# Kernel tuning notes

Hardware: AMD Instinct MI355X
Metric: run time of the kernel (lower is better)

Reference implementation:

```python
import jax, jax.numpy as jnp
import numpy as np

CIN, COUT, K = 64, 64, 3
ALPHA = 8.3
STRIDE, PAD, DIL = 1, 1, 1
B, H = 8, 128


def _unfold(x, k, dilation, padding, stride):
    # torch.nn.functional.unfold: output feature order is (C, kh, kw)
    x = jnp.pad(x, ((0, 0), (0, 0), (padding, padding), (padding, padding)))
    b, c, h, w = x.shape
    eff = dilation * (k - 1) + 1
    oh = (h - eff) // stride + 1
    ow = (w - eff) // stride + 1
    cols = []
    for i in range(k):
        for j in range(k):
            cols.append(x[:, :, i * dilation:i * dilation + stride * oh:stride,
                              j * dilation:j * dilation + stride * ow:stride])
    p = jnp.stack(cols, axis=2)          # [B, C, k*k, oh, ow]
    return p.reshape(b, c * k * k, oh * ow)


def setup_inputs() -> dict:
    key = jax.random.key(0)
    k1, k2, k3, k4 = jax.random.split(key, 4)
    image = jax.random.normal(k1, (B, CIN, H, H), dtype=jnp.float32)
    depth = jax.random.uniform(k2, (B, 1, H, H), dtype=jnp.float32)
    weight = jax.random.normal(k3, (COUT, CIN, K, K), dtype=jnp.float32) * 0.05
    bias = jax.random.normal(k4, (COUT,), dtype=jnp.float32) * 0.05
    return {"image": image, "depth": depth, "weight": weight, "bias": bias}


def reference(image, depth, weight, bias):
    # im2col of the image: [B, L, Cin*k*k]
    patches = _unfold(image, K, DIL, PAD, STRIDE).transpose(0, 2, 1)
    b, L, _ = patches.shape
    # depth is repeat()'d to Cin channels in the original; the unfolded depth
    # columns therefore tile the single-channel patch Cin times. Exploit that:
    dpatch = _unfold(depth, K, DIL, PAD, STRIDE).transpose(0, 2, 1)  # [B, L, k*k]
    # original centre index: int((Cin*k*k)/2); within the tiled patch this is
    # position (Cin*k*k//2) % (k*k) of the single-channel patch
    centre_idx = (CIN * K * K // 2) % (K * K)
    centre = dpatch[:, :, centre_idx:centre_idx + 1]
    sim = jnp.exp(-ALPHA * jnp.abs(dpatch - centre))  # [B, L, k*k]
    # modulate per kernel offset (broadcast over channels == tiled similarity)
    modulated = patches.reshape(b, L, CIN, K * K) * sim[:, :, None, :]
    out = jnp.einsum('blck,ock->blo', modulated, weight.reshape(COUT, CIN, K * K))
    out = out + bias
    osz = (image.shape[-1] + 2 * PAD - DIL * (K - 1) - 1) // STRIDE + 1
    return out.transpose(0, 2, 1).reshape(b, COUT, osz, osz)
```

## Files before the change

### kernel.cpp

```cpp
#include <hip/hip_runtime.h>
#include <hip/hip_bf16.h>

#define BATCH 8
#define CIN   64
#define COUT  64
#define HH    128
#define WW    128
#define HW    (HH * WW)
#define ALPHA 8.3f
#define TPX   64
#define YPB   2
#define XW    66

typedef __attribute__((ext_vector_type(8))) short short8;
typedef __attribute__((ext_vector_type(4))) float f32x4;

__device__ __forceinline__ int img_idx(int r, int x, int c) {
    return (((r * XW + x) << 6) + c) ^ ((x & 7) << 3);
}

__global__ __launch_bounds__(256)
void transpose_w(const float* __restrict__ w, __hip_bfloat16* __restrict__ wt) {
    int i = blockIdx.x * 256 + threadIdx.x;
    if (i >= 9 * 64 * 64) return;
    int c = i & 63;
    int o = (i >> 6) & 63;
    int tap = i >> 12;
    wt[i] = __float2bfloat16(w[(o * 64 + c) * 9 + tap]);
}

__global__ __launch_bounds__(256)
void depthconv_fused(const float* __restrict__ image,
                     const float* __restrict__ depth,
                     const float* __restrict__ bias,
                     const short* __restrict__ wt,
                     float* __restrict__ out) {
    __shared__ short s_img[4 * XW * 64];
    __shared__ float s_d[4][XW];
    __shared__ float s_sim[YPB][9][TPX];

    const int tid = threadIdx.x;
    const int bid = blockIdx.x;
    const int yg = bid & 63;
    const int xt = (bid >> 6) & 1;
    const int b  = bid >> 7;
    const int x0 = xt * TPX;
    const int y0 = yg * YPB;

    const int lane = tid & 63;
    const int wid  = tid >> 6;
    const int l15  = lane & 15;
    const int lq   = lane >> 4;
    const int o_base = wid * 16;

    short8 wfrag[9][2];
    #pragma unroll
    for (int tap = 0; tap < 9; ++tap)
        #pragma unroll
        for (int h = 0; h < 2; ++h)
            wfrag[tap][h] = *(const short8*)&wt[(tap * 64 + o_base + l15) * 64 + h * 32 + lq * 8];

    float bias_v[4];
    #pragma unroll
    for (int r = 0; r < 4; ++r) bias_v[r] = bias[o_base + lq * 4 + r];

    {
        const int sx  = 1 + (tid & 63);
        const int srr = tid >> 6;
        const int gy  = y0 - 1 + srr;
        const int gx  = x0 + (tid & 63);
        const bool yok = (unsigned)gy < HH;
        const float* ip = &image[((b * CIN) * HH + gy) * WW + gx];
        const int base = (srr * XW + sx) << 6;
        const int swz  = (sx & 7) << 3;
        #pragma unroll 16
        for (int c2 = 0; c2 < 32; ++c2) {
            float v0 = 0.f, v1 = 0.f;
            if (yok) { v0 = ip[0]; v1 = ip[HW]; }
            ip += 2 * HW;
            __hip_bfloat162 pk = __float22bfloat162_rn(float2{v0, v1});
            *(__hip_bfloat162*)&s_img[base + ((2 * c2) ^ swz)] = pk;
        }
    }
    {
        const int e   = tid & 1;
        const int sx  = e ? (XW - 1) : 0;
        const int rr  = (tid >> 1) & 3;
        const int c2  = tid >> 3;
        const int gy  = y0 - 1 + rr;
        const int gx  = x0 - 1 + sx;
        float v0 = 0.f, v1 = 0.f;
        if ((unsigned)gy < HH && (unsigned)gx < WW) {
            const float* p = &image[((b * CIN + 2 * c2) * HH + gy) * WW + gx];
            v0 = p[0]; v1 = p[HW];
        }
        __hip_bfloat162 pk = __float22bfloat162_rn(float2{v0, v1});
        *(__hip_bfloat162*)&s_img[img_idx(rr, sx, 2 * c2)] = pk;
    }
    for (int i = tid; i < 4 * XW; i += 256) {
        int rr = i / XW, x = i - rr * XW;
        int gy = y0 - 1 + rr, gx = x0 - 1 + x;
        float v = 0.f;
        if ((unsigned)gy < HH && (unsigned)gx < WW)
            v = depth[(b * HH + gy) * WW + gx];
        s_d[rr][x] = v;
    }
    __syncthreads();

    for (int i = tid; i < YPB * 9 * TPX; i += 256) {
        int p  = i & 63;
        int t  = i >> 6;
        int yy = t / 9, tap = t - yy * 9;
        int ri = tap / 3, dj = tap - ri * 3;
        float dt = s_d[yy + ri][p + dj];
        float dc = s_d[yy][p];
        s_sim[yy][tap][p] = __expf(-ALPHA * fabsf(dt - dc));
    }
    __syncthreads();

    #pragma unroll
    for (int nt = 0; nt < 4; ++nt) {
        const int xb = nt * 16 + l15;
        f32x4 a0 = f32x4{0.f, 0.f, 0.f, 0.f};
        f32x4 a1 = f32x4{0.f, 0.f, 0.f, 0.f};

        #pragma unroll
        for (int r = 0; r < 4; ++r) {
            short8 bb[3][2];
            #pragma unroll
            for (int dj = 0; dj < 3; ++dj) {
                bb[dj][0] = *(const short8*)&s_img[img_idx(r, xb + dj, lq * 8)];
                bb[dj][1] = *(const short8*)&s_img[img_idx(r, xb + dj, 32 + lq * 8)];
            }
            if (r < 3) {
                #pragma unroll
                for (int dj = 0; dj < 3; ++dj) {
                    const int tap = 3 * r + dj;
                    f32x4 tmp = __builtin_amdgcn_mfma_f32_16x16x32_bf16(
                        wfrag[tap][0], bb[dj][0], (f32x4){0.f, 0.f, 0.f, 0.f}, 0, 0, 0);
                    tmp = __builtin_amdgcn_mfma_f32_16x16x32_bf16(
                        wfrag[tap][1], bb[dj][1], tmp, 0, 0, 0);
                    const float sv = s_sim[0][tap][xb];
                    #pragma unroll
                    for (int e = 0; e < 4; ++e) a0[e] = fmaf(sv, tmp[e], a0[e]);
                }
            }
            if (r >= 1) {
                #pragma unroll
                for (int dj = 0; dj < 3; ++dj) {
                    const int tap = 3 * (r - 1) + dj;
                    f32x4 tmp = __builtin_amdgcn_mfma_f32_16x16x32_bf16(
                        wfrag[tap][0], bb[dj][0], (f32x4){0.f, 0.f, 0.f, 0.f}, 0, 0, 0);
                    tmp = __builtin_amdgcn_mfma_f32_16x16x32_bf16(
                        wfrag[tap][1], bb[dj][1], tmp, 0, 0, 0);
                    const float sv = s_sim[1][tap][xb];
                    #pragma unroll
                    for (int e = 0; e < 4; ++e) a1[e] = fmaf(sv, tmp[e], a1[e]);
                }
            }
        }

        const int px = x0 + xb;
        #pragma unroll
        for (int rr = 0; rr < 4; ++rr) {
            const int o = o_base + lq * 4 + rr;
            out[((b * COUT + o) * HH + y0) * WW + px]     = a0[rr] + bias_v[rr];
            out[((b * COUT + o) * HH + y0 + 1) * WW + px] = a1[rr] + bias_v[rr];
        }
    }
}

extern "C" void kernel_launch(void* const* d_in, const int* in_sizes, int n_in,
                              void* d_out, int out_size, void* d_ws, size_t ws_size,
                              hipStream_t stream) {
    const float* image  = (const float*)d_in[0];
    const float* depth  = (const float*)d_in[1];
    const float* weight = (const float*)d_in[2];
    const float* bias   = (const float*)d_in[3];
    float* out = (float*)d_out;
    __hip_bfloat16* wt = (__hip_bfloat16*)d_ws;

    transpose_w<<<(9 * 64 * 64 + 255) / 256, 256, 0, stream>>>(weight, wt);

    dim3 grid(BATCH * (HH / YPB) * (WW / TPX));
    depthconv_fused<<<grid, 256, 0, stream>>>(image, depth, bias,
                                              (const short*)wt, out);
}
```

Before: 121.5 us.

## Pre-transpose image to padded NHWC bf16 in workspace and read B-fragments from global

A new prep kernel converts the NCHW fp32 image into a zero-padded channels-last bf16 tensor in workspace, fused with the weight transpose in one launch. The main kernel drops its LDS image staging and reads MFMA B-fragments directly from this global buffer as contiguous 16-byte loads. This removes strided NCHW gathers and shared-memory writes from the main kernel, but adds a full extra pass over the image and relies on L2/cache for the overlapping row reuse across blocks.

```diff
diff --git a/kernel.cpp b/kernel.cpp
--- a/kernel.cpp
+++ b/kernel.cpp
@@ -11,31 +11,61 @@
 #define TPX   64
 #define YPB   2
 #define XW    66
+#define YP    (HH + 2)
+#define XP    (WW + 2)
+
+#define IMGT_SHORTS (BATCH * YP * XP * 64)
+#define WS_NEED_B   ((IMGT_SHORTS + 9 * 64 * 64) * 2)
 
 typedef __attribute__((ext_vector_type(8))) short short8;
 typedef __attribute__((ext_vector_type(4))) float f32x4;
 
-__device__ __forceinline__ int img_idx(int r, int x, int c) {
-    return (((r * XW + x) << 6) + c) ^ ((x & 7) << 3);
+__global__ __launch_bounds__(256)
+void prep(const float* __restrict__ image, const float* __restrict__ weight,
+          __hip_bfloat16* __restrict__ ws) {
+    const int bid = blockIdx.x, tid = threadIdx.x;
+    if (bid < BATCH * YP) {
+        const int b = bid / YP, yp = bid - b * YP;
+        __hip_bfloat16* row = ws + (size_t)(b * YP + yp) * XP * 64;
+        if (yp == 0 || yp == YP - 1) {
+            uint2* p = (uint2*)row;
+            for (int j = tid; j < XP * 64 / 4; j += 256) p[j] = uint2{0u, 0u};
+        } else {
+            __shared__ __hip_bfloat16 s[WW][66];
+            const int gy = yp - 1;
+            const int c0 = tid >> 7;
+            const int gx = tid & 127;
+            const float* ip = image + ((size_t)(b * CIN + c0) * HH + gy) * WW + gx;
+            #pragma unroll
+            for (int cc = 0; cc < 32; ++cc) {
+                s[gx][cc * 2 + c0] = __float2bfloat16(ip[0]);
+                ip += 2 * HW;
+            }
+            __syncthreads();
+            if (tid < 64) {
+                const int e = tid >> 5, cp = (tid & 31) * 2;
+                ((unsigned*)row)[((e ? (XP - 1) : 0) * 64 + cp) >> 1] = 0u;
+            }
+            for (int j = tid; j < WW * 64 / 2; j += 256) {
+                const int o = j * 2;
+                const int xl = o >> 6, c = o & 63;
+                unsigned v = *(const unsigned*)&s[xl][c];
+                *(unsigned*)&row[64 + o] = v;
+            }
+        }
+    } else {
+        const int i = (bid - BATCH * YP) * 256 + tid;
+        const int c = i & 63, o = (i >> 6) & 63, tap = i >> 12;
+        ws[IMGT_SHORTS + i] = __float2bfloat16(weight[(o * 64 + c) * 9 + tap]);
+    }
 }
 
 __global__ __launch_bounds__(256)
-void transpose_w(const float* __restrict__ w, __hip_bfloat16* __restrict__ wt) {
-    int i = blockIdx.x * 256 + threadIdx.x;
-    if (i >= 9 * 64 * 64) return;
-    int c = i & 63;
-    int o = (i >> 6) & 63;
-    int tap = i >> 12;
-    wt[i] = __float2bfloat16(w[(o * 64 + c) * 9 + tap]);
-}
-
-__global__ __launch_bounds__(256)
-void depthconv_fused(const float* __restrict__ image,
-                     const float* __restrict__ depth,
-                     const float* __restrict__ bias,
-                     const short* __restrict__ wt,
-                     float* __restrict__ out) {
-    __shared__ short s_img[4 * XW * 64];
+void depthconv_main(const short* __restrict__ imgT,
+                    const float* __restrict__ depth,
+                    const float* __restrict__ bias,
+                    const short* __restrict__ wt,
+                    float* __restrict__ out) {
     __shared__ float s_d[4][XW];
     __shared__ float s_sim[YPB][9][TPX];
 
@@ -64,39 +94,6 @@
     #pragma unroll
     for (int r = 0; r < 4; ++r) bias_v[r] = bias[o_base + lq * 4 + r];
 
-    {
-        const int sx  = 1 + (tid & 63);
-        const int srr = tid >> 6;
-        const int gy  = y0 - 1 + srr;
-        const int gx  = x0 + (tid & 63);
-        const bool yok = (unsigned)gy < HH;
-        const float* ip = &image[((b * CIN) * HH + gy) * WW + gx];
-        const int base = (srr * XW + sx) << 6;
-        const int swz  = (sx & 7) << 3;
-        #pragma unroll 16
-        for (int c2 = 0; c2 < 32; ++c2) {
-            float v0 = 0.f, v1 = 0.f;
-            if (yok) { v0 = ip[0]; v1 = ip[HW]; }
-            ip += 2 * HW;
-            __hip_bfloat162 pk = __float22bfloat162_rn(float2{v0, v1});
-            *(__hip_bfloat162*)&s_img[base + ((2 * c2) ^ swz)] = pk;
-        }
-    }
-    {
-        const int e   = tid & 1;
-        const int sx  = e ? (XW - 1) : 0;
-        const int rr  = (tid >> 1) & 3;
-        const int c2  = tid >> 3;
-        const int gy  = y0 - 1 + rr;
-        const int gx  = x0 - 1 + sx;
-        float v0 = 0.f, v1 = 0.f;
-        if ((unsigned)gy < HH && (unsigned)gx < WW) {
-            const float* p = &image[((b * CIN + 2 * c2) * HH + gy) * WW + gx];
-            v0 = p[0]; v1 = p[HW];
-        }
-        __hip_bfloat162 pk = __float22bfloat162_rn(float2{v0, v1});
-        *(__hip_bfloat162*)&s_img[img_idx(rr, sx, 2 * c2)] = pk;
-    }
     for (int i = tid; i < 4 * XW; i += 256) {
         int rr = i / XW, x = i - rr * XW;
         int gy = y0 - 1 + rr, gx = x0 - 1 + x;
@@ -106,7 +103,6 @@
         s_d[rr][x] = v;
     }
     __syncthreads();
-
     for (int i = tid; i < YPB * 9 * TPX; i += 256) {
         int p  = i & 63;
         int t  = i >> 6;
@@ -121,6 +117,7 @@
     #pragma unroll
     for (int nt = 0; nt < 4; ++nt) {
         const int xb = nt * 16 + l15;
+        const short* p = imgT + ((size_t)(b * YP + y0) * XP + (x0 + xb)) * 64 + lq * 8;
         f32x4 a0 = f32x4{0.f, 0.f, 0.f, 0.f};
         f32x4 a1 = f32x4{0.f, 0.f, 0.f, 0.f};
 
@@ -129,8 +126,8 @@
             short8 bb[3][2];
             #pragma unroll
             for (int dj = 0; dj < 3; ++dj) {
-                bb[dj][0] = *(const short8*)&s_img[img_idx(r, xb + dj, lq * 8)];
-                bb[dj][1] = *(const short8*)&s_img[img_idx(r, xb + dj, 32 + lq * 8)];
+                bb[dj][0] = *(const short8*)(p + dj * 64);
+                bb[dj][1] = *(const short8*)(p + dj * 64 + 32);
             }
             if (r < 3) {
                 #pragma unroll
@@ -158,6 +155,7 @@
                     for (int e = 0; e < 4; ++e) a1[e] = fmaf(sv, tmp[e], a1[e]);
                 }
             }
+            p += XP * 64;
         }
 
         const int px = x0 + xb;
@@ -178,11 +176,11 @@
     const float* weight = (const float*)d_in[2];
     const float* bias   = (const float*)d_in[3];
     float* out = (float*)d_out;
-    __hip_bfloat16* wt = (__hip_bfloat16*)d_ws;
+    __hip_bfloat16* ws = (__hip_bfloat16*)d_ws;
 
-    transpose_w<<<(9 * 64 * 64 + 255) / 256, 256, 0, stream>>>(weight, wt);
+    prep<<<BATCH * YP + (9 * 64 * 64) / 256, 256, 0, stream>>>(image, weight, ws);
 
     dim3 grid(BATCH * (HH / YPB) * (WW / TPX));
-    depthconv_fused<<<grid, 256, 0, stream>>>(image, depth, bias,
-                                              (const short*)wt, out);
+    depthconv_main<<<grid, 256, 0, stream>>>((const short*)ws, depth, bias,
+                                             (const short*)ws + IMGT_SHORTS, out);
 }
```

Measured after the change: 145.5 us. 19.8% more time.

## Process four output rows per block and prefetch extra halo rows into registers

Applied to the files above, without the earlier changes.

Each block now computes four output rows instead of two, so the one-row halo above and below is shared across more outputs and the redundant image rows loaded into LDS drop. The two extra input rows are loaded into registers before the first compute pass and written to shared memory only after it, overlapping that global load latency with MFMA work. Global loads also become unconditional, with out-of-range values masked afterward. In exchange the grid halves to 512 blocks, LDS use grows, and the 32 staged floats per thread raise register pressure, which may reduce occupancy.

```diff
diff --git a/kernel.cpp b/kernel.cpp
--- a/kernel.cpp
+++ b/kernel.cpp
@@ -9,7 +9,6 @@
 #define HW    (HH * WW)
 #define ALPHA 8.3f
 #define TPX   64
-#define YPB   2
 #define XW    66
 
 typedef __attribute__((ext_vector_type(8))) short short8;
@@ -35,17 +34,17 @@
                      const float* __restrict__ bias,
                      const short* __restrict__ wt,
                      float* __restrict__ out) {
-    __shared__ short s_img[4 * XW * 64];
-    __shared__ float s_d[4][XW];
-    __shared__ float s_sim[YPB][9][TPX];
+    __shared__ short s_img[6 * XW * 64];
+    __shared__ float s_d[6][XW];
+    __shared__ float s_sim[4][9][TPX];
 
     const int tid = threadIdx.x;
     const int bid = blockIdx.x;
-    const int yg = bid & 63;
-    const int xt = (bid >> 6) & 1;
-    const int b  = bid >> 7;
+    const int yg = bid & 31;
+    const int xt = (bid >> 5) & 1;
+    const int b  = bid >> 6;
     const int x0 = xt * TPX;
-    const int y0 = yg * YPB;
+    const int y0 = yg * 4;
 
     const int lane = tid & 63;
     const int wid  = tid >> 6;
@@ -70,13 +69,13 @@
         const int gy  = y0 - 1 + srr;
         const int gx  = x0 + (tid & 63);
         const bool yok = (unsigned)gy < HH;
-        const float* ip = &image[((b * CIN) * HH + gy) * WW + gx];
+        const float* ip = &image[((b * CIN) * HH + (yok ? gy : 0)) * WW + gx];
         const int base = (srr * XW + sx) << 6;
         const int swz  = (sx & 7) << 3;
         #pragma unroll 16
         for (int c2 = 0; c2 < 32; ++c2) {
-            float v0 = 0.f, v1 = 0.f;
-            if (yok) { v0 = ip[0]; v1 = ip[HW]; }
+            float v0 = ip[0], v1 = ip[HW];
+            if (!yok) { v0 = 0.f; v1 = 0.f; }
             ip += 2 * HW;
             __hip_bfloat162 pk = __float22bfloat162_rn(float2{v0, v1});
             *(__hip_bfloat162*)&s_img[base + ((2 * c2) ^ swz)] = pk;
@@ -97,7 +96,7 @@
         __hip_bfloat162 pk = __float22bfloat162_rn(float2{v0, v1});
         *(__hip_bfloat162*)&s_img[img_idx(rr, sx, 2 * c2)] = pk;
     }
-    for (int i = tid; i < 4 * XW; i += 256) {
+    for (int i = tid; i < 6 * XW; i += 256) {
         int rr = i / XW, x = i - rr * XW;
         int gy = y0 - 1 + rr, gx = x0 - 1 + x;
         float v = 0.f;
@@ -105,9 +104,35 @@
             v = depth[(b * HH + gy) * WW + gx];
         s_d[rr][x] = v;
     }
+
+    float st[32];
+    float st_e;
+    const int r45  = 4 + (tid >> 7);
+    const int sx45 = 1 + ((tid >> 1) & 63);
+    const int ch0  = (tid & 1) * 32;
+    {
+        const int gy  = y0 - 1 + r45;
+        const bool ok = (unsigned)gy < HH;
+        const int gx  = x0 + ((tid >> 1) & 63);
+        const float* ip = &image[((size_t)(b * CIN + ch0) * HH + (ok ? gy : 0)) * WW + gx];
+        #pragma unroll
+        for (int c = 0; c < 32; ++c) {
+            float v = ip[0];
+            st[c] = ok ? v : 0.f;
+            ip += HW;
+        }
+        const int ee  = (tid >> 6) & 1;
+        const int ec  = tid & 63;
+        const int gye = y0 - 1 + r45;
+        const int gxe = x0 - 1 + (ee ? 65 : 0);
+        const bool oke = (unsigned)gye < HH && (unsigned)gxe < WW;
+        const float* pe = &image[((size_t)(b * CIN + ec) * HH + (oke ? gye : 0)) * WW + (oke ? gxe : 0)];
+        float ve = pe[0];
+        st_e = oke ? ve : 0.f;
+    }
     __syncthreads();
 
-    for (int i = tid; i < YPB * 9 * TPX; i += 256) {
+    for (int i = tid; i < 4 * 9 * TPX; i += 256) {
         int p  = i & 63;
         int t  = i >> 6;
         int yy = t / 9, tap = t - yy * 9;
@@ -118,56 +143,77 @@
     }
     __syncthreads();
 
-    #pragma unroll
-    for (int nt = 0; nt < 4; ++nt) {
-        const int xb = nt * 16 + l15;
-        f32x4 a0 = f32x4{0.f, 0.f, 0.f, 0.f};
-        f32x4 a1 = f32x4{0.f, 0.f, 0.f, 0.f};
-
-        #pragma unroll
-        for (int r = 0; r < 4; ++r) {
-            short8 bb[3][2];
+    auto compute_pair = [&](const int p) {
+        #pragma unroll
+        for (int nt = 0; nt < 4; ++nt) {
+            const int xb = nt * 16 + l15;
+            f32x4 a0 = f32x4{0.f, 0.f, 0.f, 0.f};
+            f32x4 a1 = f32x4{0.f, 0.f, 0.f, 0.f};
             #pragma unroll
-            for (int dj = 0; dj < 3; ++dj) {
-                bb[dj][0] = *(const short8*)&s_img[img_idx(r, xb + dj, lq * 8)];
-                bb[dj][1] = *(const short8*)&s_img[img_idx(r, xb + dj, 32 + lq * 8)];
-            }
-            if (r < 3) {
+            for (int r = 0; r < 4; ++r) {
+                const int rr = 2 * p + r;
+                short8 bb[3][2];
                 #pragma unroll
                 for (int dj = 0; dj < 3; ++dj) {
-                    const int tap = 3 * r + dj;
-                    f32x4 tmp = __builtin_amdgcn_mfma_f32_16x16x32_bf16(
-                        wfrag[tap][0], bb[dj][0], (f32x4){0.f, 0.f, 0.f, 0.f}, 0, 0, 0);
-                    tmp = __builtin_amdgcn_mfma_f32_16x16x32_bf16(
-                        wfrag[tap][1], bb[dj][1], tmp, 0, 0, 0);
-                    const float sv = s_sim[0][tap][xb];
+                    bb[dj][0] = *(const short8*)&s_img[img_idx(rr, xb + dj, lq * 8)];
+                    bb[dj][1] = *(const short8*)&s_img[img_idx(rr, xb + dj, 32 + lq * 8)];
+                }
+                if (r < 3) {
                     #pragma unroll
-                    for (int e = 0; e < 4; ++e) a0[e] = fmaf(sv, tmp[e], a0[e]);
+                    for (int dj = 0; dj < 3; ++dj) {
+                        const int tap = 3 * r + dj;
+                        f32x4 tmp = __builtin_amdgcn_mfma_f32_16x16x32_bf16(
+                            wfrag[tap][0], bb[dj][0], (f32x4){0.f, 0.f, 0.f, 0.f}, 0, 0, 0);
+                        tmp = __builtin_amdgcn_mfma_f32_16x16x32_bf16(
+                            wfrag[tap][1], bb[dj][1], tmp, 0, 0, 0);
+                        const float sv = s_sim[2 * p][tap][xb];
+                        #pragma unroll
+                        for (int e = 0; e < 4; ++e) a0[e] = fmaf(sv, tmp[e], a0[e]);
+                    }
+                }
+                if (r >= 1) {
+                    #pragma unroll
+                    for (int dj = 0; dj < 3; ++dj) {
+                        const int tap = 3 * (r - 1) + dj;
+                        f32x4 tmp = __builtin_amdgcn_mfma_f32_16x16x32_bf16(
+                            wfrag[tap][0], bb[dj][0], (f32x4){0.f, 0.f, 0.f, 0.f}, 0, 0, 0);
+                        tmp = __builtin_amdgcn_mfma_f32_16x16x32_bf16(
+                            wfrag[tap][1], bb[dj][1], tmp, 0, 0, 0);
+                        const float sv = s_sim[2 * p + 1][tap][xb];
+                        #pragma unroll
+                        for (int e = 0; e < 4; ++e) a1[e] = fmaf(sv, tmp[e], a1[e]);
+                    }
                 }
             }
-            if (r >= 1) {
-                #pragma unroll
-                for (int dj = 0; dj < 3; ++dj) {
-                    const int tap = 3 * (r - 1) + dj;
-                    f32x4 tmp = __builtin_amdgcn_mfma_f32_16x16x32_bf16(
-                        wfrag[tap][0], bb[dj][0], (f32x4){0.f, 0.f, 0.f, 0.f}, 0, 0, 0);
-                    tmp = __builtin_amdgcn_mfma_f32_16x16x32_bf16(
-                        wfrag[tap][1], bb[dj][1], tmp, 0, 0, 0);
-                    const float sv = s_sim[1][tap][xb];
-                    #pragma unroll
-                    for (int e = 0; e < 4; ++e) a1[e] = fmaf(sv, tmp[e], a1[e]);
-                }
+            const int px = x0 + xb;
+            const int yb = y0 + 2 * p;
+            #pragma unroll
+            for (int rr = 0; rr < 4; ++rr) {
+                const int o = o_base + lq * 4 + rr;
+                out[((b * COUT + o) * HH + yb) * WW + px]     = a0[rr] + bias_v[rr];
+                out[((b * COUT + o) * HH + yb + 1) * WW + px] = a1[rr] + bias_v[rr];
             }
         }
-
-        const int px = x0 + xb;
-        #pragma unroll
-        for (int rr = 0; rr < 4; ++rr) {
-            const int o = o_base + lq * 4 + rr;
-            out[((b * COUT + o) * HH + y0) * WW + px]     = a0[rr] + bias_v[rr];
-            out[((b * COUT + o) * HH + y0 + 1) * WW + px] = a1[rr] + bias_v[rr];
-        }
-    }
+    };
+
+    compute_pair(0);
+
+    {
+        const int base = ((r45 * XW + sx45) << 6) + ch0;
+        const int swz  = (sx45 & 7) << 3;
+        #pragma unroll
+        for (int c2 = 0; c2 < 16; ++c2) {
+            __hip_bfloat162 pk = __float22bfloat162_rn(float2{st[2 * c2], st[2 * c2 + 1]});
+            *(__hip_bfloat162*)&s_img[(base + 2 * c2) ^ swz] = pk;
+        }
+        const int ee = (tid >> 6) & 1;
+        const int ec = tid & 63;
+        s_img[img_idx(r45, ee ? (XW - 1) : 0, ec)] =
+            __builtin_bit_cast(short, __float2bfloat16(st_e));
+    }
+    __syncthreads();
+
+    compute_pair(1);
 }
 
 extern "C" void kernel_launch(void* const* d_in, const int* in_sizes, int n_in,
@@ -182,7 +228,7 @@
 
     transpose_w<<<(9 * 64 * 64 + 255) / 256, 256, 0, stream>>>(weight, wt);
 
-    dim3 grid(BATCH * (HH / YPB) * (WW / TPX));
+    dim3 grid(BATCH * 2 * 32);
     depthconv_fused<<<grid, 256, 0, stream>>>(image, depth, bias,
                                               (const short*)wt, out);
 }
```

After: 113.4 us. 6.7% less time.

## Process four output rows per block with 512 threads and warp-specialized loads

Applied to the files above, without the earlier changes.

Each block now covers four output rows instead of two, using eight waves split into two row groups, each handling four output-channel groups. The six-row image halo tile is shared across the row groups, cutting redundant global reads of halo rows. Loading is specialized by wave: six waves load rows, one loads edge columns, one loads depth. The weight fragment load moves after the first barrier. The cost is larger LDS use, fewer blocks, and a serialized edge-column load on only 12 lanes.

```diff
diff --git a/kernel.cpp b/kernel.cpp
--- a/kernel.cpp
+++ b/kernel.cpp
@@ -9,7 +9,6 @@
 #define HW    (HH * WW)
 #define ALPHA 8.3f
 #define TPX   64
-#define YPB   2
 #define XW    66
 
 typedef __attribute__((ext_vector_type(8))) short short8;
@@ -29,29 +28,86 @@
     wt[i] = __float2bfloat16(w[(o * 64 + c) * 9 + tap]);
 }
 
-__global__ __launch_bounds__(256)
+__global__ __launch_bounds__(512)
 void depthconv_fused(const float* __restrict__ image,
                      const float* __restrict__ depth,
                      const float* __restrict__ bias,
                      const short* __restrict__ wt,
                      float* __restrict__ out) {
-    __shared__ short s_img[4 * XW * 64];
-    __shared__ float s_d[4][XW];
-    __shared__ float s_sim[YPB][9][TPX];
+    __shared__ short s_img[6 * XW * 64];
+    __shared__ float s_d[6][XW];
+    __shared__ float s_sim[4][9][TPX];
 
     const int tid = threadIdx.x;
     const int bid = blockIdx.x;
-    const int yg = bid & 63;
-    const int xt = (bid >> 6) & 1;
-    const int b  = bid >> 7;
+    const int yg = bid & 31;
+    const int xt = (bid >> 5) & 1;
+    const int b  = bid >> 6;
     const int x0 = xt * TPX;
-    const int y0 = yg * YPB;
+    const int y0 = yg * 4;
 
     const int lane = tid & 63;
     const int wid  = tid >> 6;
     const int l15  = lane & 15;
     const int lq   = lane >> 4;
-    const int o_base = wid * 16;
+    const int og   = wid & 3;
+    const int pr   = wid >> 2;
+    const int o_base = og * 16;
+
+    if (wid < 6) {
+        const int sx  = 1 + lane;
+        const int gy  = y0 - 1 + wid;
+        const bool yok = (unsigned)gy < HH;
+        const int gx  = x0 + lane;
+        const float* ip = &image[((b * CIN) * HH + (yok ? gy : 0)) * WW + gx];
+        const int base = (wid * XW + sx) << 6;
+        const int swz  = (sx & 7) << 3;
+        #pragma unroll 16
+        for (int c2 = 0; c2 < 32; ++c2) {
+            float v0 = ip[0], v1 = ip[HW];
+            if (!yok) { v0 = 0.f; v1 = 0.f; }
+            ip += 2 * HW;
+            __hip_bfloat162 pk = __float22bfloat162_rn(float2{v0, v1});
+            *(__hip_bfloat162*)&s_img[base + ((2 * c2) ^ swz)] = pk;
+        }
+    } else if (wid == 6) {
+        if (lane < 12) {
+            const int rr = lane >> 1, e = lane & 1;
+            const int sx = e ? (XW - 1) : 0;
+            const int gy = y0 - 1 + rr;
+            const int gx = x0 - 1 + sx;
+            const bool ok = (unsigned)gy < HH && (unsigned)gx < WW;
+            const float* p = &image[((b * CIN) * HH + (ok ? gy : 0)) * WW + (ok ? gx : 0)];
+            #pragma unroll 8
+            for (int c2 = 0; c2 < 32; ++c2) {
+                float v0 = p[0], v1 = p[HW];
+                if (!ok) { v0 = 0.f; v1 = 0.f; }
+                p += 2 * HW;
+                __hip_bfloat162 pk = __float22bfloat162_rn(float2{v0, v1});
+                *(__hip_bfloat162*)&s_img[img_idx(rr, sx, 2 * c2)] = pk;
+            }
+        }
+    } else {
+        for (int i = lane; i < 6 * XW; i += 64) {
+            int rr = i / XW, x = i - rr * XW;
+            int gy = y0 - 1 + rr, gx = x0 - 1 + x;
+            float v = 0.f;
+            if ((unsigned)gy < HH && (unsigned)gx < WW)
+                v = depth[(b * HH + gy) * WW + gx];
+            s_d[rr][x] = v;
+        }
+    }
+    __syncthreads();
+
+    for (int i = tid; i < 4 * 9 * TPX; i += 512) {
+        int p  = i & 63;
+        int t  = i >> 6;
+        int yy = t / 9, tap = t - yy * 9;
+        int ri = tap / 3, dj = tap - ri * 3;
+        float dt = s_d[yy + ri][p + dj];
+        float dc = s_d[yy][p];
+        s_sim[yy][tap][p] = __expf(-ALPHA * fabsf(dt - dc));
+    }
 
     short8 wfrag[9][2];
     #pragma unroll
@@ -64,58 +120,6 @@
     #pragma unroll
     for (int r = 0; r < 4; ++r) bias_v[r] = bias[o_base + lq * 4 + r];
 
-    {
-        const int sx  = 1 + (tid & 63);
-        const int srr = tid >> 6;
-        const int gy  = y0 - 1 + srr;
-        const int gx  = x0 + (tid & 63);
-        const bool yok = (unsigned)gy < HH;
-        const float* ip = &image[((b * CIN) * HH + gy) * WW + gx];
-        const int base = (srr * XW + sx) << 6;
-        const int swz  = (sx & 7) << 3;
-        #pragma unroll 16
-        for (int c2 = 0; c2 < 32; ++c2) {
-            float v0 = 0.f, v1 = 0.f;
-            if (yok) { v0 = ip[0]; v1 = ip[HW]; }
-            ip += 2 * HW;
-            __hip_bfloat162 pk = __float22bfloat162_rn(float2{v0, v1});
-            *(__hip_bfloat162*)&s_img[base + ((2 * c2) ^ swz)] = pk;
-        }
-    }
-    {
-        const int e   = tid & 1;
-        const int sx  = e ? (XW - 1) : 0;
-        const int rr  = (tid >> 1) & 3;
-        const int c2  = tid >> 3;
-        const int gy  = y0 - 1 + rr;
-        const int gx  = x0 - 1 + sx;
-        float v0 = 0.f, v1 = 0.f;
-        if ((unsigned)gy < HH && (unsigned)gx < WW) {
-            const float* p = &image[((b * CIN + 2 * c2) * HH + gy) * WW + gx];
-            v0 = p[0]; v1 = p[HW];
-        }
-        __hip_bfloat162 pk = __float22bfloat162_rn(float2{v0, v1});
-        *(__hip_bfloat162*)&s_img[img_idx(rr, sx, 2 * c2)] = pk;
-    }
-    for (int i = tid; i < 4 * XW; i += 256) {
-        int rr = i / XW, x = i - rr * XW;
-        int gy = y0 - 1 + rr, gx = x0 - 1 + x;
-        float v = 0.f;
-        if ((unsigned)gy < HH && (unsigned)gx < WW)
-            v = depth[(b * HH + gy) * WW + gx];
-        s_d[rr][x] = v;
-    }
-    __syncthreads();
-
-    for (int i = tid; i < YPB * 9 * TPX; i += 256) {
-        int p  = i & 63;
-        int t  = i >> 6;
-        int yy = t / 9, tap = t - yy * 9;
-        int ri = tap / 3, dj = tap - ri * 3;
-        float dt = s_d[yy + ri][p + dj];
-        float dc = s_d[yy][p];
-        s_sim[yy][tap][p] = __expf(-ALPHA * fabsf(dt - dc));
-    }
     __syncthreads();
 
     #pragma unroll
@@ -123,14 +127,14 @@
         const int xb = nt * 16 + l15;
         f32x4 a0 = f32x4{0.f, 0.f, 0.f, 0.f};
         f32x4 a1 = f32x4{0.f, 0.f, 0.f, 0.f};
-
         #pragma unroll
         for (int r = 0; r < 4; ++r) {
+            const int rr = 2 * pr + r;
             short8 bb[3][2];
             #pragma unroll
             for (int dj = 0; dj < 3; ++dj) {
-                bb[dj][0] = *(const short8*)&s_img[img_idx(r, xb + dj, lq * 8)];
-                bb[dj][1] = *(const short8*)&s_img[img_idx(r, xb + dj, 32 + lq * 8)];
+                bb[dj][0] = *(const short8*)&s_img[img_idx(rr, xb + dj, lq * 8)];
+                bb[dj][1] = *(const short8*)&s_img[img_idx(rr, xb + dj, 32 + lq * 8)];
             }
             if (r < 3) {
                 #pragma unroll
@@ -140,7 +144,7 @@
                         wfrag[tap][0], bb[dj][0], (f32x4){0.f, 0.f, 0.f, 0.f}, 0, 0, 0);
                     tmp = __builtin_amdgcn_mfma_f32_16x16x32_bf16(
                         wfrag[tap][1], bb[dj][1], tmp, 0, 0, 0);
-                    const float sv = s_sim[0][tap][xb];
+                    const float sv = s_sim[2 * pr][tap][xb];
                     #pragma unroll
                     for (int e = 0; e < 4; ++e) a0[e] = fmaf(sv, tmp[e], a0[e]);
                 }
@@ -153,19 +157,19 @@
                         wfrag[tap][0], bb[dj][0], (f32x4){0.f, 0.f, 0.f, 0.f}, 0, 0, 0);
                     tmp = __builtin_amdgcn_mfma_f32_16x16x32_bf16(
                         wfrag[tap][1], bb[dj][1], tmp, 0, 0, 0);
-                    const float sv = s_sim[1][tap][xb];
+                    const float sv = s_sim[2 * pr + 1][tap][xb];
                     #pragma unroll
                     for (int e = 0; e < 4; ++e) a1[e] = fmaf(sv, tmp[e], a1[e]);
                 }
             }
         }
-
         const int px = x0 + xb;
+        const int yb = y0 + 2 * pr;
         #pragma unroll
         for (int rr = 0; rr < 4; ++rr) {
             const int o = o_base + lq * 4 + rr;
-            out[((b * COUT + o) * HH + y0) * WW + px]     = a0[rr] + bias_v[rr];
-            out[((b * COUT + o) * HH + y0 + 1) * WW + px] = a1[rr] + bias_v[rr];
+            out[((b * COUT + o) * HH + yb) * WW + px]     = a0[rr] + bias_v[rr];
+            out[((b * COUT + o) * HH + yb + 1) * WW + px] = a1[rr] + bias_v[rr];
         }
     }
 }
@@ -182,7 +186,7 @@
 
     transpose_w<<<(9 * 64 * 64 + 255) / 256, 256, 0, stream>>>(weight, wt);
 
-    dim3 grid(BATCH * (HH / YPB) * (WW / TPX));
-    depthconv_fused<<<grid, 256, 0, stream>>>(image, depth, bias,
+    dim3 grid(BATCH * 2 * 32);
+    depthconv_fused<<<grid, 512, 0, stream>>>(image, depth, bias,
                                               (const short*)wt, out);
 }
```

Result: faster. 110.4 us (-9.2%).
